# Performance work log

Hardware: AMD Instinct MI355X
Metric: run time of the kernel (lower is better)

The kernel has to match this reference:

```python
import jax, jax.numpy as jnp
import numpy as np

B, S, T, D = 4, 512, 512, 256


def setup_inputs() -> dict:
    key = jax.random.key(0)
    ks = jax.random.split(key, 10)
    scale = 1.0 / np.sqrt(D)
    return {
        "source": jax.random.normal(ks[0], (B, S, D), jnp.float32),
        "target": jax.random.normal(ks[1], (B, T, D), jnp.float32),
        "W_src": jax.random.uniform(ks[2], (D, D), jnp.float32, -scale, scale),
        "b_src": jax.random.uniform(ks[3], (D,), jnp.float32, -scale, scale),
        "W_tgt": jax.random.uniform(ks[4], (D, D), jnp.float32, -scale, scale),
        "b_tgt": jax.random.uniform(ks[5], (D,), jnp.float32, -scale, scale),
        "W_res": jax.random.uniform(ks[6], (D, 1), jnp.float32, -scale, scale),
        "b_res": jax.random.uniform(ks[7], (1,), jnp.float32, -scale, scale),
        "W_prob": jax.random.uniform(ks[8], (D, 2), jnp.float32, -scale, scale),
        "b_prob": jax.random.uniform(ks[9], (2,), jnp.float32, -scale, scale),
    }


def reference(source, target, W_src, b_src, W_tgt, b_tgt, W_res, b_res, W_prob, b_prob):
    # source: (B,S,D), target: (B,T,D)
    src_lin = jnp.einsum("bsd,de->bse", source, W_src) + b_src  # (B,S,D)
    tgt_lin = jnp.einsum("btd,de->bte", target, W_tgt) + b_tgt  # (B,T,D)
    # Bahdanau-style additive attention: (B,T,S,D) broadcast, tanh, D->1
    h = jnp.tanh(src_lin[:, None, :, :] + tgt_lin[:, :, None, :])  # (B,T,S,D)
    genP = jnp.einsum("btsd,d->bts", h, W_res[:, 0]) + b_res[0]     # (B,T,S)
    prob = jax.nn.softmax(jnp.einsum("btd,de->bte", target, W_prob) + b_prob, axis=-1)  # (B,T,2)
    return genP, prob
```

## Files before the change

### kernel.cpp

```cpp
#include <hip/hip_runtime.h>

#define B_ 4
#define S_ 512
#define T_ 512
#define D_ 256
#define NSRC (B_ * S_)
#define K2F 2.8853900817779268f

typedef __attribute__((ext_vector_type(8))) short short8;
typedef __attribute__((ext_vector_type(4))) float f32x4;
typedef __attribute__((ext_vector_type(2))) float f32x2;

__device__ __forceinline__ unsigned short f2bf(float f) {
    union { float f; unsigned u; } v; v.f = f;
    unsigned r = v.u + 0x7FFF + ((v.u >> 16) & 1);
    return (unsigned short)(r >> 16);
}

__global__ __launch_bounds__(256) void prep_kernel(
    const float* __restrict__ src, const float* __restrict__ tgt,
    const float* __restrict__ Wsrc, const float* __restrict__ Wtgt,
    const float* __restrict__ Wp, const float* __restrict__ bp,
    unsigned short* __restrict__ abf, unsigned short* __restrict__ wtb,
    float* __restrict__ out)
{
    __shared__ float tl[64 * 65];
    const int blk = blockIdx.x, tid = threadIdx.x;

    if (blk < 1024) {
        int i4 = blk * 256 + tid;
        const int half = NSRC * D_ / 4;
        const float4* in = (i4 < half) ? (const float4*)src : (const float4*)tgt;
        int j = (i4 < half) ? i4 : i4 - half;
        float4 v = in[j];
        ushort4 o;
        o.x = f2bf(v.x); o.y = f2bf(v.y); o.z = f2bf(v.z); o.w = f2bf(v.w);
        *(ushort4*)&abf[i4 * 4] = o;
    } else if (blk < 1056) {
        int wb = blk - 1024;
        int e = wb >> 4, ti = wb & 15, tr = ti >> 2, tc = ti & 3;
        int r0 = tr * 64, c0 = tc * 64;
        const float* W = e ? Wtgt : Wsrc;
        #pragma unroll
        for (int it = 0; it < 4; it++) {
            int rr = (tid >> 4) + it * 16;
            int cc = (tid & 15) * 4;
            float4 v = *(const float4*)&W[(r0 + rr) * D_ + c0 + cc];
            tl[(cc + 0) * 65 + rr] = v.x;
            tl[(cc + 1) * 65 + rr] = v.y;
            tl[(cc + 2) * 65 + rr] = v.z;
            tl[(cc + 3) * 65 + rr] = v.w;
        }
        __syncthreads();
        #pragma unroll
        for (int it = 0; it < 2; it++) {
            int jj = (tid >> 3) + it * 32;
            int kk = (tid & 7) * 8;
            ushort4 lo, hi;
            lo.x = f2bf(tl[jj * 65 + kk + 0]); lo.y = f2bf(tl[jj * 65 + kk + 1]);
            lo.z = f2bf(tl[jj * 65 + kk + 2]); lo.w = f2bf(tl[jj * 65 + kk + 3]);
            hi.x = f2bf(tl[jj * 65 + kk + 4]); hi.y = f2bf(tl[jj * 65 + kk + 5]);
            hi.z = f2bf(tl[jj * 65 + kk + 6]); hi.w = f2bf(tl[jj * 65 + kk + 7]);
            int idx = (e * 256 + c0 + jj) * D_ + r0 + kk;
            *(ushort4*)&wtb[idx] = lo;
            *(ushort4*)&wtb[idx + 4] = hi;
        }
    } else {
        int row  = (blk - 1056) * 4 + (tid >> 6);
        int lane = tid & 63;
        float p0 = 0.f, p1 = 0.f;
        #pragma unroll
        for (int i = 0; i < 4; i++) {
            int d = lane + i * 64;
            float v = tgt[row * D_ + d];
            float2 w = *(const float2*)&Wp[d * 2];
            p0 = fmaf(v, w.x, p0);
            p1 = fmaf(v, w.y, p1);
        }
        #pragma unroll
        for (int off = 32; off > 0; off >>= 1) {
            p0 += __shfl_down(p0, off, 64);
            p1 += __shfl_down(p1, off, 64);
        }
        if (lane == 0) {
            const float L2E = 1.4426950408889634f;
            float l0 = p0 + bp[0], l1 = p1 + bp[1];
            float e10 = __builtin_amdgcn_exp2f((l1 - l0) * L2E);
            float e01 = __builtin_amdgcn_exp2f((l0 - l1) * L2E);
            out[B_ * T_ * S_ + row * 2 + 0] = __builtin_amdgcn_rcpf(1.f + e10);
            out[B_ * T_ * S_ + row * 2 + 1] = __builtin_amdgcn_rcpf(1.f + e01);
        }
    }
}

#define LSTR 68
__global__ __launch_bounds__(768, 1) void mega_kernel(
    const unsigned short* __restrict__ abf, const unsigned short* __restrict__ wtb,
    const float* __restrict__ bsrc, const float* __restrict__ btgt,
    const float* __restrict__ Wres, const float* __restrict__ bres,
    float* __restrict__ out)
{
    __shared__ float ls[2][64 * LSTR];
    __shared__ float lt[2][64 * LSTR];
    __shared__ float c0s;

    const int tid = threadIdx.x;
    const int lane = tid & 63, w = tid >> 6;
    const int s0 = blockIdx.x * 64;
    const int t0 = blockIdx.y * 64;
    const int b  = blockIdx.z;

    if (w == 0) {
        float s = Wres[lane] + Wres[lane + 64] + Wres[lane + 128] + Wres[lane + 192];
        #pragma unroll
        for (int off = 32; off > 0; off >>= 1) s += __shfl_xor(s, off, 64);
        if (lane == 0) c0s = s + bres[0];
    }

    const bool producer = (w < 4);

    const int pw  = w & 3;
    const int mat = pw >> 1;
    const int rb  = 2 * (pw & 1);
    const int n = lane & 15, quad = lane >> 4;
    const float* bias = mat ? btgt : bsrc;
    const unsigned short* wtbase = wtb + mat * 256 * D_;
    const int R0 = mat ? (NSRC + b * T_ + t0) : (b * S_ + s0);

    short8 af[2][8];
    if (producer) {
        #pragma unroll
        for (int rg = 0; rg < 2; rg++)
            #pragma unroll
            for (int ks = 0; ks < 8; ks++)
                af[rg][ks] = *(const short8*)&abf[(R0 + (rb + rg) * 16 + n) * D_ + ks * 32 + quad * 8];
    }

    auto phaseA = [&](int c, int bi) {
        float* lx = (mat ? lt[bi] : ls[bi]);
        #pragma unroll
        for (int cg = 0; cg < 4; cg++) {
            const int gcol = c * 4 + cg;
            const unsigned short* bptr = &wtbase[(gcol * 16 + n) * D_ + quad * 8];
            short8 bf[8];
            #pragma unroll
            for (int ks = 0; ks < 8; ks++) bf[ks] = *(const short8*)&bptr[ks * 32];
            const int dloc = cg * 16 + n;
            const float bv = bias[gcol * 16 + n];
            #pragma unroll
            for (int rg = 0; rg < 2; rg++) {
                f32x4 a4 = {0.f, 0.f, 0.f, 0.f};
                #pragma unroll
                for (int ks = 0; ks < 8; ks++)
                    a4 = __builtin_amdgcn_mfma_f32_16x16x32_bf16(af[rg][ks], bf[ks], a4, 0, 0, 0);
                float4 o;
                o.x = __builtin_amdgcn_exp2f((a4[0] + bv) * K2F);
                o.y = __builtin_amdgcn_exp2f((a4[1] + bv) * K2F);
                o.z = __builtin_amdgcn_exp2f((a4[2] + bv) * K2F);
                o.w = __builtin_amdgcn_exp2f((a4[3] + bv) * K2F);
                *(float4*)&lx[dloc * LSTR + (rb + rg) * 16 + quad * 4] = o;
            }
        }
    };

    const int cl = tid - 256;
    const int m = cl & 15;
    const int g = cl >> 4;
    f32x2 acc[2][2];
    #pragma unroll
    for (int i = 0; i < 2; i++) {
        acc[i][0] = (f32x2){0.f, 0.f};
        acc[i][1] = (f32x2){0.f, 0.f};
    }

    if (producer) phaseA(0, 0);
    __syncthreads();

    for (int c = 0; c < 4; c++) {
        const int bi = c & 1;
        if (producer) {
            if (c < 3) phaseA(c + 1, bi ^ 1);
        } else {
            const float* lsb = ls[bi];
            const float* ltb = lt[bi];
            const float* wp = &Wres[c * 64];
            const f32x2 one2 = {1.f, 1.f};
            #pragma unroll 4
            for (int kq = 0; kq < 16; kq++) {
                const int d0 = 4 * kq;
                float4 av0 = *(const float4*)&lsb[(d0 + 0) * LSTR + 4 * m];
                float4 av1 = *(const float4*)&lsb[(d0 + 1) * LSTR + 4 * m];
                float4 av2 = *(const float4*)&lsb[(d0 + 2) * LSTR + 4 * m];
                float4 av3 = *(const float4*)&lsb[(d0 + 3) * LSTR + 4 * m];
                float2 cv0 = *(const float2*)&ltb[(d0 + 0) * LSTR + 2 * g];
                float2 cv1 = *(const float2*)&ltb[(d0 + 1) * LSTR + 2 * g];
                float2 cv2 = *(const float2*)&ltb[(d0 + 2) * LSTR + 2 * g];
                float2 cv3 = *(const float2*)&ltb[(d0 + 3) * LSTR + 2 * g];
                const float w0 = wp[d0], w1 = wp[d0 + 1];
                const float w2 = wp[d0 + 2], w3 = wp[d0 + 3];
                const f32x2 w0v = {w0, w0}, w1v = {w1, w1};
                const f32x2 w2v = {w2, w2}, w3v = {w3, w3};
                f32x2 a0p[2] = {{av0.x, av0.y}, {av0.z, av0.w}};
                f32x2 a1p[2] = {{av1.x, av1.y}, {av1.z, av1.w}};
                f32x2 a2p[2] = {{av2.x, av2.y}, {av2.z, av2.w}};
                f32x2 a3p[2] = {{av3.x, av3.y}, {av3.z, av3.w}};
                const float cc0[2] = {cv0.x, cv0.y};
                const float cc1[2] = {cv1.x, cv1.y};
                const float cc2[2] = {cv2.x, cv2.y};
                const float cc3[2] = {cv3.x, cv3.y};
                #pragma unroll
                for (int i = 0; i < 2; i++) {
                    const f32x2 c0v = {cc0[i], cc0[i]};
                    const f32x2 c1v = {cc1[i], cc1[i]};
                    const f32x2 c2v = {cc2[i], cc2[i]};
                    const f32x2 c3v = {cc3[i], cc3[i]};
                    #pragma unroll
                    for (int jp = 0; jp < 2; jp++) {
                        f32x2 dd0 = a0p[jp] * c0v + one2;
                        f32x2 dd1 = a1p[jp] * c1v + one2;
                        f32x2 dd2 = a2p[jp] * c2v + one2;
                        f32x2 dd3 = a3p[jp] * c3v + one2;
                        f32x2 p01 = dd0 * dd1;
                        f32x2 p23 = dd2 * dd3;
                        f32x2 den = p01 * p23;
                        f32x2 u01 = dd1 * w0v;
                        u01 = dd0 * w1v + u01;
                        f32x2 u23 = dd3 * w2v;
                        u23 = dd2 * w3v + u23;
                        f32x2 num = u01 * p23;
                        num = u23 * p01 + num;
                        f32x2 r;
                        r.x = __builtin_amdgcn_rcpf(den.x);
                        r.y = __builtin_amdgcn_rcpf(den.y);
                        acc[i][jp] = num * r + acc[i][jp];
                    }
                }
            }
        }
        __syncthreads();
    }

    if (!producer) {
        const float C0 = c0s;
        #pragma unroll
        for (int i = 0; i < 2; i++) {
            float4 o;
            o.x = C0 - 2.f * acc[i][0].x;
            o.y = C0 - 2.f * acc[i][0].y;
            o.z = C0 - 2.f * acc[i][1].x;
            o.w = C0 - 2.f * acc[i][1].y;
            *(float4*)&out[(b * T_ + t0 + 2 * g + i) * S_ + s0 + 4 * m] = o;
        }
    }
}

extern "C" void kernel_launch(void* const* d_in, const int* in_sizes, int n_in,
                              void* d_out, int out_size, void* d_ws, size_t ws_size,
                              hipStream_t stream) {
    const float* source = (const float*)d_in[0];
    const float* target = (const float*)d_in[1];
    const float* W_src  = (const float*)d_in[2];
    const float* b_src  = (const float*)d_in[3];
    const float* W_tgt  = (const float*)d_in[4];
    const float* b_tgt  = (const float*)d_in[5];
    const float* W_res  = (const float*)d_in[6];
    const float* b_res  = (const float*)d_in[7];
    const float* W_prob = (const float*)d_in[8];
    const float* b_prob = (const float*)d_in[9];
    float* out = (float*)d_out;

    unsigned short* abf = (unsigned short*)d_ws;
    unsigned short* wtb = abf + 2 * NSRC * D_;

    prep_kernel<<<1568, 256, 0, stream>>>(source, target, W_src, W_tgt,
                                          W_prob, b_prob, abf, wtb, out);
    mega_kernel<<<dim3(8, 8, 4), 768, 0, stream>>>(abf, wtb, b_src, b_tgt,
                                                   W_res, b_res, out);
}
```

Baseline: 108.0 us.

## Convert activations to bf16 inside mega kernel and batch eight tanh terms per reciprocal

Removes the separate bf16 conversion pass over source/target in the prep kernel; producers now load fp32 activations directly and convert in registers. This drops a global write and re-read of the bf16 copies, but each mega block re-reads fp32 rows, twice the bytes, and the same rows are loaded redundantly across blocks. The consumer loop now combines eight rational tanh terms over a common denominator per reciprocal instead of four, halving rcp instructions at the cost of more register pressure and a larger product that risks overflow or precision loss.

```diff
diff --git a/kernel.cpp b/kernel.cpp
--- a/kernel.cpp
+++ b/kernel.cpp
@@ -18,26 +18,16 @@
 }
 
 __global__ __launch_bounds__(256) void prep_kernel(
-    const float* __restrict__ src, const float* __restrict__ tgt,
+    const float* __restrict__ tgt,
     const float* __restrict__ Wsrc, const float* __restrict__ Wtgt,
     const float* __restrict__ Wp, const float* __restrict__ bp,
-    unsigned short* __restrict__ abf, unsigned short* __restrict__ wtb,
-    float* __restrict__ out)
+    unsigned short* __restrict__ wtb, float* __restrict__ out)
 {
     __shared__ float tl[64 * 65];
     const int blk = blockIdx.x, tid = threadIdx.x;
 
-    if (blk < 1024) {
-        int i4 = blk * 256 + tid;
-        const int half = NSRC * D_ / 4;
-        const float4* in = (i4 < half) ? (const float4*)src : (const float4*)tgt;
-        int j = (i4 < half) ? i4 : i4 - half;
-        float4 v = in[j];
-        ushort4 o;
-        o.x = f2bf(v.x); o.y = f2bf(v.y); o.z = f2bf(v.z); o.w = f2bf(v.w);
-        *(ushort4*)&abf[i4 * 4] = o;
-    } else if (blk < 1056) {
-        int wb = blk - 1024;
+    if (blk < 32) {
+        int wb = blk;
         int e = wb >> 4, ti = wb & 15, tr = ti >> 2, tc = ti & 3;
         int r0 = tr * 64, c0 = tc * 64;
         const float* W = e ? Wtgt : Wsrc;
@@ -66,7 +56,7 @@
             *(ushort4*)&wtb[idx + 4] = hi;
         }
     } else {
-        int row  = (blk - 1056) * 4 + (tid >> 6);
+        int row  = (blk - 32) * 4 + (tid >> 6);
         int lane = tid & 63;
         float p0 = 0.f, p1 = 0.f;
         #pragma unroll
@@ -95,7 +85,8 @@
 
 #define LSTR 68
 __global__ __launch_bounds__(768, 1) void mega_kernel(
-    const unsigned short* __restrict__ abf, const unsigned short* __restrict__ wtb,
+    const float* __restrict__ src, const float* __restrict__ tgt,
+    const unsigned short* __restrict__ wtb,
     const float* __restrict__ bsrc, const float* __restrict__ btgt,
     const float* __restrict__ Wres, const float* __restrict__ bres,
     float* __restrict__ out)
@@ -125,15 +116,24 @@
     const int n = lane & 15, quad = lane >> 4;
     const float* bias = mat ? btgt : bsrc;
     const unsigned short* wtbase = wtb + mat * 256 * D_;
-    const int R0 = mat ? (NSRC + b * T_ + t0) : (b * S_ + s0);
 
     short8 af[2][8];
     if (producer) {
+        const float* xb = mat ? &tgt[(b * T_ + t0) * D_] : &src[(b * S_ + s0) * D_];
         #pragma unroll
         for (int rg = 0; rg < 2; rg++)
             #pragma unroll
-            for (int ks = 0; ks < 8; ks++)
-                af[rg][ks] = *(const short8*)&abf[(R0 + (rb + rg) * 16 + n) * D_ + ks * 32 + quad * 8];
+            for (int ks = 0; ks < 8; ks++) {
+                const float* p = &xb[((rb + rg) * 16 + n) * D_ + ks * 32 + quad * 8];
+                float4 u0 = *(const float4*)p;
+                float4 u1 = *(const float4*)(p + 4);
+                short8 v;
+                v[0] = (short)f2bf(u0.x); v[1] = (short)f2bf(u0.y);
+                v[2] = (short)f2bf(u0.z); v[3] = (short)f2bf(u0.w);
+                v[4] = (short)f2bf(u1.x); v[5] = (short)f2bf(u1.y);
+                v[6] = (short)f2bf(u1.z); v[7] = (short)f2bf(u1.w);
+                af[rg][ks] = v;
+            }
     }
 
     auto phaseA = [&](int c, int bi) {
@@ -185,50 +185,46 @@
             const float* ltb = lt[bi];
             const float* wp = &Wres[c * 64];
             const f32x2 one2 = {1.f, 1.f};
-            #pragma unroll 4
-            for (int kq = 0; kq < 16; kq++) {
-                const int d0 = 4 * kq;
-                float4 av0 = *(const float4*)&lsb[(d0 + 0) * LSTR + 4 * m];
-                float4 av1 = *(const float4*)&lsb[(d0 + 1) * LSTR + 4 * m];
-                float4 av2 = *(const float4*)&lsb[(d0 + 2) * LSTR + 4 * m];
-                float4 av3 = *(const float4*)&lsb[(d0 + 3) * LSTR + 4 * m];
-                float2 cv0 = *(const float2*)&ltb[(d0 + 0) * LSTR + 2 * g];
-                float2 cv1 = *(const float2*)&ltb[(d0 + 1) * LSTR + 2 * g];
-                float2 cv2 = *(const float2*)&ltb[(d0 + 2) * LSTR + 2 * g];
-                float2 cv3 = *(const float2*)&ltb[(d0 + 3) * LSTR + 2 * g];
-                const float w0 = wp[d0], w1 = wp[d0 + 1];
-                const float w2 = wp[d0 + 2], w3 = wp[d0 + 3];
-                const f32x2 w0v = {w0, w0}, w1v = {w1, w1};
-                const f32x2 w2v = {w2, w2}, w3v = {w3, w3};
-                f32x2 a0p[2] = {{av0.x, av0.y}, {av0.z, av0.w}};
-                f32x2 a1p[2] = {{av1.x, av1.y}, {av1.z, av1.w}};
-                f32x2 a2p[2] = {{av2.x, av2.y}, {av2.z, av2.w}};
-                f32x2 a3p[2] = {{av3.x, av3.y}, {av3.z, av3.w}};
-                const float cc0[2] = {cv0.x, cv0.y};
-                const float cc1[2] = {cv1.x, cv1.y};
-                const float cc2[2] = {cv2.x, cv2.y};
-                const float cc3[2] = {cv3.x, cv3.y};
+            #pragma unroll 2
+            for (int kq = 0; kq < 8; kq++) {
+                const int d0 = 8 * kq;
+                f32x2 ap[8][2];
+                float cc[8][2];
+                f32x2 wv[8];
+                #pragma unroll
+                for (int k = 0; k < 8; k++) {
+                    float4 a4 = *(const float4*)&lsb[(d0 + k) * LSTR + 4 * m];
+                    float2 c2 = *(const float2*)&ltb[(d0 + k) * LSTR + 2 * g];
+                    ap[k][0] = (f32x2){a4.x, a4.y};
+                    ap[k][1] = (f32x2){a4.z, a4.w};
+                    cc[k][0] = c2.x; cc[k][1] = c2.y;
+                    const float wk = wp[d0 + k];
+                    wv[k] = (f32x2){wk, wk};
+                }
                 #pragma unroll
                 for (int i = 0; i < 2; i++) {
-                    const f32x2 c0v = {cc0[i], cc0[i]};
-                    const f32x2 c1v = {cc1[i], cc1[i]};
-                    const f32x2 c2v = {cc2[i], cc2[i]};
-                    const f32x2 c3v = {cc3[i], cc3[i]};
                     #pragma unroll
                     for (int jp = 0; jp < 2; jp++) {
-                        f32x2 dd0 = a0p[jp] * c0v + one2;
-                        f32x2 dd1 = a1p[jp] * c1v + one2;
-                        f32x2 dd2 = a2p[jp] * c2v + one2;
-                        f32x2 dd3 = a3p[jp] * c3v + one2;
-                        f32x2 p01 = dd0 * dd1;
-                        f32x2 p23 = dd2 * dd3;
-                        f32x2 den = p01 * p23;
-                        f32x2 u01 = dd1 * w0v;
-                        u01 = dd0 * w1v + u01;
-                        f32x2 u23 = dd3 * w2v;
-                        u23 = dd2 * w3v + u23;
-                        f32x2 num = u01 * p23;
-                        num = u23 * p01 + num;
+                        f32x2 dd[8];
+                        #pragma unroll
+                        for (int k = 0; k < 8; k++) {
+                            const f32x2 cs = {cc[k][i], cc[k][i]};
+                            dd[k] = ap[k][jp] * cs + one2;
+                        }
+                        f32x2 p01 = dd[0] * dd[1];
+                        f32x2 p23 = dd[2] * dd[3];
+                        f32x2 p45 = dd[4] * dd[5];
+                        f32x2 p67 = dd[6] * dd[7];
+                        f32x2 q03 = p01 * p23;
+                        f32x2 q47 = p45 * p67;
+                        f32x2 den = q03 * q47;
+                        f32x2 u01 = dd[1] * wv[0]; u01 = dd[0] * wv[1] + u01;
+                        f32x2 u23 = dd[3] * wv[2]; u23 = dd[2] * wv[3] + u23;
+                        f32x2 u45 = dd[5] * wv[4]; u45 = dd[4] * wv[5] + u45;
+                        f32x2 u67 = dd[7] * wv[6]; u67 = dd[6] * wv[7] + u67;
+                        f32x2 n03 = u01 * p23; n03 = u23 * p01 + n03;
+                        f32x2 n47 = u45 * p67; n47 = u67 * p45 + n47;
+                        f32x2 num = n03 * q47; num = n47 * q03 + num;
                         f32x2 r;
                         r.x = __builtin_amdgcn_rcpf(den.x);
                         r.y = __builtin_amdgcn_rcpf(den.y);
@@ -269,11 +265,11 @@
     const float* b_prob = (const float*)d_in[9];
     float* out = (float*)d_out;
 
-    unsigned short* abf = (unsigned short*)d_ws;
-    unsigned short* wtb = abf + 2 * NSRC * D_;
-
-    prep_kernel<<<1568, 256, 0, stream>>>(source, target, W_src, W_tgt,
-                                          W_prob, b_prob, abf, wtb, out);
-    mega_kernel<<<dim3(8, 8, 4), 768, 0, stream>>>(abf, wtb, b_src, b_tgt,
+    unsigned short* wtb = (unsigned short*)d_ws;
+
+    prep_kernel<<<544, 256, 0, stream>>>(target, W_src, W_tgt,
+                                         W_prob, b_prob, wtb, out);
+    mega_kernel<<<dim3(8, 8, 4), 768, 0, stream>>>(source, target, wtb,
+                                                   b_src, b_tgt,
                                                    W_res, b_res, out);
 }
```

After: 107.6 us. Within noise of the previous version (-0.4%).
